# Kernel optimization log

Measured on AMD Instinct MI355X. Metric: run time of the kernel, lower is better.

Reference implementation:

```python
import jax, jax.numpy as jnp
import numpy as np

N_NODES = 50000
N_EDGES = 800000
IN_CH = 64
EDGE_DIM = 8
HIDDEN = 128
NUM_GRAPHS = 256


def setup_inputs() -> dict:
    key = jax.random.key(0)
    ks = jax.random.split(key, 16)
    x = jax.random.normal(ks[0], (N_NODES, IN_CH), dtype=jnp.float32)
    edge_index = jax.random.randint(ks[1], (2, N_EDGES), 0, N_NODES, dtype=jnp.int64)
    edge_attr = jax.random.normal(ks[2], (N_EDGES, EDGE_DIM), dtype=jnp.float32)
    batch = jnp.sort(jax.random.randint(ks[3], (N_NODES,), 0, NUM_GRAPHS, dtype=jnp.int64))

    def lin(k, fan_in, fan_out):
        bound = 1.0 / np.sqrt(fan_in)
        kw, kb = jax.random.split(k)
        W = jax.random.uniform(kw, (fan_in, fan_out), minval=-bound, maxval=bound, dtype=jnp.float32)
        b = jax.random.uniform(kb, (fan_out,), minval=-bound, maxval=bound, dtype=jnp.float32)
        return W, b

    W1, b1 = lin(ks[4], IN_CH, HIDDEN)
    We1, be1 = lin(ks[5], EDGE_DIM, IN_CH)
    W2, b2 = lin(ks[6], HIDDEN, HIDDEN)
    We2, be2 = lin(ks[7], EDGE_DIM, HIDDEN)
    W3, b3 = lin(ks[8], HIDDEN, HIDDEN)
    We3, be3 = lin(ks[9], EDGE_DIM, HIDDEN)
    return {"x": x, "edge_index": edge_index, "edge_attr": edge_attr, "batch": batch,
            "W1": W1, "b1": b1, "We1": We1, "be1": be1,
            "W2": W2, "b2": b2, "We2": We2, "be2": be2,
            "W3": W3, "b3": b3, "We3": We3, "be3": be3}


def gine_conv(x, src, dst, edge_attr, W, b, We, be):
    # edge feature projection to node-feature dim, then message = relu(x_j + e)
    e = edge_attr @ We + be                      # [E, d]
    msg = jax.nn.relu(x[src] + e)                # [E, d]
    agg = jax.ops.segment_sum(msg, dst, num_segments=x.shape[0])  # [N, d]
    # eps = 0 (PyG default, not trainable)
    return (x + agg) @ W + b


def reference(x, edge_index, edge_attr, batch,
              W1, b1, We1, be1, W2, b2, We2, be2, W3, b3, We3, be3):
    x = x.astype(jnp.float32)
    edge_attr = edge_attr.astype(jnp.float32)
    src, dst = edge_index[0], edge_index[1]
    x = jax.nn.relu(gine_conv(x, src, dst, edge_attr, W1, b1, We1, be1))
    x = jax.nn.relu(gine_conv(x, src, dst, edge_attr, W2, b2, We2, be2))
    x = jax.nn.relu(gine_conv(x, src, dst, edge_attr, W3, b3, We3, be3))
    # global mean pool over graphs
    sums = jax.ops.segment_sum(x, batch, num_segments=NUM_GRAPHS)          # [G, d]
    counts = jax.ops.segment_sum(jnp.ones((x.shape[0],), x.dtype), batch, num_segments=NUM_GRAPHS)
    return sums / jnp.maximum(counts, 1.0)[:, None]
```

## Files before the change

### kernel.cpp

```cpp
#include <hip/hip_runtime.h>
#include <hip/hip_bf16.h>
#include <hip/hip_fp16.h>

#define N_NODES 50000
#define N_EDGES 800000
#define IN_CH 64
#define EDGE_DIM 8
#define HIDDEN 128
#define NUM_GRAPHS 256
#define QSCALE 256.0f
#define QINV   (1.0f / 256.0f)

typedef __attribute__((ext_vector_type(8))) _Float16 half8;
typedef __attribute__((ext_vector_type(4))) float floatx4;
typedef __attribute__((ext_vector_type(2))) float floatx2;
typedef __attribute__((ext_vector_type(4))) int intx4;

static __device__ __forceinline__ __half2 u2h(int u) {
    union { int i; __half2 h; } cv; cv.i = u; return cv.h;
}
static __device__ __forceinline__ int h2u(__half2 h) {
    union { __half2 h; int i; } cv; cv.h = h; return cv.i;
}
static __device__ __forceinline__ unsigned short h1u(__half h) {
    union { __half h; unsigned short u; } cv; cv.h = h; return cv.u;
}
static __device__ __forceinline__ unsigned char f32_to_fp8(float v) {
    int pk = __builtin_amdgcn_cvt_pk_fp8_f32(v, v, 0, false);
    return (unsigned char)(pk & 0xff);
}

#define XH_ELEMS (N_NODES * IN_CH)

__global__ __launch_bounds__(256) void hist_cvt_kernel(
    const int* __restrict__ dst, int* __restrict__ deg,
    const float* __restrict__ x, unsigned char* __restrict__ xh8,
    const float* __restrict__ W1, const float* __restrict__ W2,
    const float* __restrict__ W3,
    _Float16* __restrict__ Wt1, _Float16* __restrict__ Wt2,
    _Float16* __restrict__ Wt3, int E)
{
    int i = blockIdx.x * blockDim.x + threadIdx.x;
    if (i < E) atomicAdd(&deg[dst[i]], 1);
    int idx = i;
    if (idx < XH_ELEMS) { xh8[idx] = f32_to_fp8(x[idx]); return; }
    idx -= XH_ELEMS;
    if (idx < 128 * IN_CH) {
        int n = idx / IN_CH, k = idx - n * IN_CH;
        Wt1[idx] = (_Float16)W1[k * 128 + n];
        return;
    }
    idx -= 128 * IN_CH;
    if (idx < 128 * HIDDEN) {
        int n = idx / HIDDEN, k = idx - n * HIDDEN;
        Wt2[idx] = (_Float16)W2[k * 128 + n];
        return;
    }
    idx -= 128 * HIDDEN;
    if (idx < 128 * HIDDEN) {
        int n = idx / HIDDEN, k = idx - n * HIDDEN;
        Wt3[idx] = (_Float16)W3[k * 128 + n];
    }
}

__global__ __launch_bounds__(256) void scan1_kernel(
    const int* __restrict__ deg, int* __restrict__ incl,
    int* __restrict__ blockSums, int N)
{
    __shared__ int s[256];
    int b = blockIdx.x, t = threadIdx.x;
    int i0 = b * 512 + 2 * t;
    int a0 = (i0 < N) ? deg[i0] : 0;
    int a1 = (i0 + 1 < N) ? deg[i0 + 1] : 0;
    int ps = a0 + a1;
    s[t] = ps;
    __syncthreads();
    for (int off = 1; off < 256; off <<= 1) {
        int v = (t >= off) ? s[t - off] : 0;
        __syncthreads();
        s[t] += v;
        __syncthreads();
    }
    int exclp = s[t] - ps;
    if (i0 < N)     incl[i0]     = exclp + a0;
    if (i0 + 1 < N) incl[i0 + 1] = exclp + a0 + a1;
    if (t == 255) blockSums[b] = s[255];
}

__global__ __launch_bounds__(128) void scan2_kernel(int* __restrict__ blockSums, int B)
{
    __shared__ int s[128];
    int t = threadIdx.x;
    int v = (t < B) ? blockSums[t] : 0;
    s[t] = v;
    __syncthreads();
    for (int off = 1; off < 128; off <<= 1) {
        int u = (t >= off) ? s[t - off] : 0;
        __syncthreads();
        s[t] += u;
        __syncthreads();
    }
    if (t < B) blockSums[t] = s[t] - v;
}

__global__ __launch_bounds__(256) void scan3_kernel(
    const int* __restrict__ incl, const int* __restrict__ deg,
    const int* __restrict__ blockSums, int* __restrict__ rowptr,
    int* __restrict__ pos, int N)
{
    int i = blockIdx.x * blockDim.x + threadIdx.x;
    if (i >= N) return;
    int v = incl[i] - deg[i] + blockSums[i >> 9];
    rowptr[i] = v;
    pos[i] = v;
}

__global__ __launch_bounds__(256) void scatter_rec_kernel(
    const int* __restrict__ dst, const int* __restrict__ src,
    const float* __restrict__ ea, int* __restrict__ pos,
    int* __restrict__ rec, int E)
{
    int e = blockIdx.x * blockDim.x + threadIdx.x;
    if (e >= E) return;
    int d = dst[e];
    int p = atomicAdd(&pos[d], 1);
    const float4* q = (const float4*)(ea + (size_t)e * EDGE_DIM);
    float4 a = q[0], b = q[1];
    intx4 r;
    r.x = src[e];
    r.y = h2u(__floats2half2_rn(a.x, a.y));
    r.z = h2u(__floats2half2_rn(a.z, a.w));
    r.w = h2u(__floats2half2_rn(b.x, b.y));
    int* rp = rec + (size_t)p * 8;
    __builtin_nontemporal_store(r, (intx4*)rp);
    __builtin_nontemporal_store(h2u(__floats2half2_rn(b.z, b.w)), rp + 4);
}

#define BF 8

__global__ __launch_bounds__(256) void gather_xs128_kernel(
    const unsigned char* __restrict__ h8,
    const int*    __restrict__ rec,
    const int*    __restrict__ rowptr,
    const int*    __restrict__ deg,
    const float*  __restrict__ We,
    const float*  __restrict__ be,
    __half*       __restrict__ xs,
    int N)
{
    int wave = threadIdx.x >> 6;
    int n    = blockIdx.x * 4 + wave;
    if (n >= N) return;
    int l  = threadIdx.x & 63;
    int j0 = 2 * l;

    __half2 hw[8];
    #pragma unroll
    for (int k = 0; k < 8; ++k) {
        float2 wv = *(const float2*)&We[k * 128 + j0];
        hw[k] = __floats2half2_rn(wv.x, wv.y);
    }
    float2 bevf = *(const float2*)&be[j0];
    __half2 bev2 = __floats2half2_rn(bevf.x, bevf.y);

    int start = __builtin_amdgcn_readfirstlane(rowptr[n]);
    int dg    = __builtin_amdgcn_readfirstlane(deg[n]);

    unsigned short selfraw = *(const unsigned short*)&h8[(size_t)n * 128 + j0];
    floatx2 hf = __builtin_amdgcn_cvt_pk_f32_fp8((int)selfraw, false);
    int acci0 = 0, acci1 = 0;

    int nb = dg / BF;
    int base = start;
    for (int b = 0; b < nb; ++b, base += BF) {
        intx4 r0[BF]; int r1[BF];
        #pragma unroll
        for (int t = 0; t < BF; ++t)
            r0[t] = __builtin_nontemporal_load(
                (const intx4*)&rec[(size_t)(base + t) * 8]);
        #pragma unroll
        for (int t = 0; t < BF; ++t)
            r1[t] = __builtin_nontemporal_load(&rec[(size_t)(base + t) * 8 + 4]);
        int sid[BF];
        #pragma unroll
        for (int t = 0; t < BF; ++t)
            sid[t] = __builtin_amdgcn_readfirstlane(r0[t].x);
        unsigned short hraw[BF];
        #pragma unroll
        for (int t = 0; t < BF; ++t)
            hraw[t] = *(const unsigned short*)&h8[(size_t)sid[t] * 128 + j0];

        #pragma unroll
        for (int t = 0; t < BF; ++t) {
            __half2 e01 = u2h(r0[t].y), e23 = u2h(r0[t].z);
            __half2 e45 = u2h(r0[t].w), e67 = u2h(r1[t]);
            __half2 m = __hfma2(__low2half2(e01),  hw[0], bev2);
            m = __hfma2(__high2half2(e01), hw[1], m);
            m = __hfma2(__low2half2(e23),  hw[2], m);
            m = __hfma2(__high2half2(e23), hw[3], m);
            m = __hfma2(__low2half2(e45),  hw[4], m);
            m = __hfma2(__high2half2(e45), hw[5], m);
            m = __hfma2(__low2half2(e67),  hw[6], m);
            m = __hfma2(__high2half2(e67), hw[7], m);
            floatx2 hs = __builtin_amdgcn_cvt_pk_f32_fp8((int)hraw[t], false);
            float m0 = __half2float(__low2half(m))  + hs.x;
            float m1 = __half2float(__high2half(m)) + hs.y;
            acci0 += (int)((m0 > 0.0f ? m0 : 0.0f) * QSCALE);
            acci1 += (int)((m1 > 0.0f ? m1 : 0.0f) * QSCALE);
        }
    }
    int end = start + dg;
    for (int idx = base; idx < end; ++idx) {
        intx4 r0 = __builtin_nontemporal_load((const intx4*)&rec[(size_t)idx * 8]);
        int r1v  = __builtin_nontemporal_load(&rec[(size_t)idx * 8 + 4]);
        int s = __builtin_amdgcn_readfirstlane(r0.x);
        unsigned short hr = *(const unsigned short*)&h8[(size_t)s * 128 + j0];
        __half2 e01 = u2h(r0.y), e23 = u2h(r0.z), e45 = u2h(r0.w), e67 = u2h(r1v);
        __half2 m = __hfma2(__low2half2(e01),  hw[0], bev2);
        m = __hfma2(__high2half2(e01), hw[1], m);
        m = __hfma2(__low2half2(e23),  hw[2], m);
        m = __hfma2(__high2half2(e23), hw[3], m);
        m = __hfma2(__low2half2(e45),  hw[4], m);
        m = __hfma2(__high2half2(e45), hw[5], m);
        m = __hfma2(__low2half2(e67),  hw[6], m);
        m = __hfma2(__high2half2(e67), hw[7], m);
        floatx2 hs = __builtin_amdgcn_cvt_pk_f32_fp8((int)hr, false);
        float m0 = __half2float(__low2half(m))  + hs.x;
        float m1 = __half2float(__high2half(m)) + hs.y;
        acci0 += (int)((m0 > 0.0f ? m0 : 0.0f) * QSCALE);
        acci1 += (int)((m1 > 0.0f ? m1 : 0.0f) * QSCALE);
    }
    float acc0 = hf.x + (float)acci0 * QINV;
    float acc1 = hf.y + (float)acci1 * QINV;
    __builtin_nontemporal_store(h2u(__floats2half2_rn(acc0, acc1)),
                                (int*)&xs[(size_t)n * 128 + j0]);
}

__global__ __launch_bounds__(256) void gather_xs64_kernel(
    const unsigned char* __restrict__ h8,
    const int*    __restrict__ rec,
    const int*    __restrict__ rowptr,
    const int*    __restrict__ deg,
    const float*  __restrict__ We,
    const float*  __restrict__ be,
    __half*       __restrict__ xs,
    int N)
{
    int wave = threadIdx.x >> 6;
    int n    = blockIdx.x * 4 + wave;
    if (n >= N) return;
    int j = threadIdx.x & 63;

    __half2 w2[4];
    #pragma unroll
    for (int p = 0; p < 4; ++p)
        w2[p] = __floats2half2_rn(We[(2 * p) * 64 + j], We[(2 * p + 1) * 64 + j]);
    float bej = be[j];

    int start = __builtin_amdgcn_readfirstlane(rowptr[n]);
    int dg    = __builtin_amdgcn_readfirstlane(deg[n]);

    float selff = __builtin_amdgcn_cvt_f32_fp8((int)h8[(size_t)n * 64 + j], 0);
    int acci = 0;

    int nb = dg / BF;
    int base = start;
    for (int b = 0; b < nb; ++b, base += BF) {
        intx4 r0[BF]; int r1[BF];
        #pragma unroll
        for (int t = 0; t < BF; ++t)
            r0[t] = __builtin_nontemporal_load(
                (const intx4*)&rec[(size_t)(base + t) * 8]);
        #pragma unroll
        for (int t = 0; t < BF; ++t)
            r1[t] = __builtin_nontemporal_load(&rec[(size_t)(base + t) * 8 + 4]);
        int sid[BF];
        #pragma unroll
        for (int t = 0; t < BF; ++t)
            sid[t] = __builtin_amdgcn_readfirstlane(r0[t].x);
        unsigned char hraw[BF];
        #pragma unroll
        for (int t = 0; t < BF; ++t)
            hraw[t] = h8[(size_t)sid[t] * 64 + j];

        #pragma unroll
        for (int t = 0; t < BF; ++t) {
            __half2 d = __hmul2(u2h(r0[t].y), w2[0]);
            d = __hfma2(u2h(r0[t].z), w2[1], d);
            d = __hfma2(u2h(r0[t].w), w2[2], d);
            d = __hfma2(u2h(r1[t]),   w2[3], d);
            float proj = __half2float(__low2half(d)) + __half2float(__high2half(d));
            float hrf = __builtin_amdgcn_cvt_f32_fp8((int)hraw[t], 0);
            float m = hrf + proj + bej;
            acci += (int)((m > 0.0f ? m : 0.0f) * QSCALE);
        }
    }
    int end = start + dg;
    for (int idx = base; idx < end; ++idx) {
        intx4 r0 = __builtin_nontemporal_load((const intx4*)&rec[(size_t)idx * 8]);
        int r1v  = __builtin_nontemporal_load(&rec[(size_t)idx * 8 + 4]);
        int s = __builtin_amdgcn_readfirstlane(r0.x);
        float hrf = __builtin_amdgcn_cvt_f32_fp8((int)h8[(size_t)s * 64 + j], 0);
        __half2 d = __hmul2(u2h(r0.y), w2[0]);
        d = __hfma2(u2h(r0.z), w2[1], d);
        d = __hfma2(u2h(r0.w), w2[2], d);
        d = __hfma2(u2h(r1v),  w2[3], d);
        float proj = __half2float(__low2half(d)) + __half2float(__high2half(d));
        float m = hrf + proj + bej;
        acci += (int)((m > 0.0f ? m : 0.0f) * QSCALE);
    }
    float acc = selff + (float)acci * QINV;
    __builtin_nontemporal_store(h1u(__float2half(acc)),
                                (unsigned short*)&xs[(size_t)n * 64 + j]);
}

template<int K, bool OUT8>
__global__ __launch_bounds__(256) void node_mfma_kernel(
    const _Float16* __restrict__ xs,
    const _Float16* __restrict__ Wt,
    const float*    __restrict__ b,
    _Float16*       __restrict__ out16,
    unsigned char*  __restrict__ out8,
    int N)
{
    int wave  = threadIdx.x >> 6;
    int lane  = threadIdx.x & 63;
    int row16 = lane & 15;
    int quad  = lane >> 4;
    int m0    = (blockIdx.x * 4 + wave) * 32;

    int nA = m0 + row16;        if (nA >= N) nA = N - 1;
    int nB = m0 + 16 + row16;   if (nB >= N) nB = N - 1;

    floatx4 accA[8], accB[8];
    #pragma unroll
    for (int t = 0; t < 8; ++t) { accA[t] = (floatx4)(0.0f); accB[t] = (floatx4)(0.0f); }

    #pragma unroll
    for (int kc = 0; kc < K; kc += 32) {
        half8 a0 = __builtin_nontemporal_load((const half8*)&xs[(size_t)nA * K + kc + quad * 8]);
        half8 a1 = __builtin_nontemporal_load((const half8*)&xs[(size_t)nB * K + kc + quad * 8]);
        #pragma unroll
        for (int t = 0; t < 8; ++t) {
            half8 bf = *(const half8*)&Wt[(size_t)(t * 16 + row16) * K + kc + quad * 8];
            accA[t] = __builtin_amdgcn_mfma_f32_16x16x32_f16(a0, bf, accA[t], 0, 0, 0);
            accB[t] = __builtin_amdgcn_mfma_f32_16x16x32_f16(a1, bf, accB[t], 0, 0, 0);
        }
    }

    #pragma unroll
    for (int t = 0; t < 8; ++t) {
        int col = t * 16 + row16;
        float bj = b[col];
        #pragma unroll
        for (int r = 0; r < 4; ++r) {
            int nodeA = m0 + quad * 4 + r;
            if (nodeA < N) {
                float v = accA[t][r] + bj;
                v = v > 0.0f ? v : 0.0f;
                if (OUT8) out8[(size_t)nodeA * 128 + col] = f32_to_fp8(v);
                else      out16[(size_t)nodeA * 128 + col] = (_Float16)v;
            }
            int nodeB = m0 + 16 + quad * 4 + r;
            if (nodeB < N) {
                float v = accB[t][r] + bj;
                v = v > 0.0f ? v : 0.0f;
                if (OUT8) out8[(size_t)nodeB * 128 + col] = f32_to_fp8(v);
                else      out16[(size_t)nodeB * 128 + col] = (_Float16)v;
            }
        }
    }
}

__global__ __launch_bounds__(256) void pool_kernel(
    const __half* __restrict__ h,
    const int*    __restrict__ batch,
    float*        __restrict__ out,
    int N)
{
    __shared__ int s_lo, s_hi;
    __shared__ float part[4][128];
    int g  = blockIdx.x;
    int t  = threadIdx.x;
    int fp = t & 63;
    int r  = t >> 6;

    if (t == 0) {
        int lo = 0, hi = N;
        while (lo < hi) { int m = (lo + hi) >> 1; if (batch[m] < g) lo = m + 1; else hi = m; }
        s_lo = lo;
        int lo2 = lo, hi2 = N;
        while (lo2 < hi2) { int m = (lo2 + hi2) >> 1; if (batch[m] < g + 1) lo2 = m + 1; else hi2 = m; }
        s_hi = lo2;
    }
    __syncthreads();

    int lo = s_lo, hi = s_hi;
    float a0 = 0.0f, a1 = 0.0f;
    for (int n = lo + r; n < hi; n += 4) {
        float2 f = __half22float2(*(const __half2*)&h[(size_t)n * 128 + 2 * fp]);
        a0 += f.x; a1 += f.y;
    }
    part[r][2 * fp]     = a0;
    part[r][2 * fp + 1] = a1;
    __syncthreads();

    if (r == 0) {
        float s0 = part[0][2 * fp] + part[1][2 * fp] + part[2][2 * fp] + part[3][2 * fp];
        float s1 = part[0][2 * fp + 1] + part[1][2 * fp + 1] + part[2][2 * fp + 1] + part[3][2 * fp + 1];
        float c = (float)(hi - lo);
        float d = c > 1.0f ? c : 1.0f;
        out[g * HIDDEN + 2 * fp]     = s0 / d;
        out[g * HIDDEN + 2 * fp + 1] = s1 / d;
    }
}

extern "C" void kernel_launch(void* const* d_in, const int* in_sizes, int n_in,
                              void* d_out, int out_size, void* d_ws, size_t ws_size,
                              hipStream_t stream)
{
    const float* x   = (const float*)d_in[0];
    const int*   ei  = (const int*)d_in[1];
    const float* ea  = (const float*)d_in[2];
    const int*   bat = (const int*)d_in[3];
    const float* W1  = (const float*)d_in[4];
    const float* b1  = (const float*)d_in[5];
    const float* We1 = (const float*)d_in[6];
    const float* be1 = (const float*)d_in[7];
    const float* W2  = (const float*)d_in[8];
    const float* b2  = (const float*)d_in[9];
    const float* We2 = (const float*)d_in[10];
    const float* be2 = (const float*)d_in[11];
    const float* W3  = (const float*)d_in[12];
    const float* b3  = (const float*)d_in[13];
    const float* We3 = (const float*)d_in[14];
    const float* be3 = (const float*)d_in[15];
    float* out = (float*)d_out;

    const int* src = ei;
    const int* dst = ei + N_EDGES;

    int* deg       = (int*)d_ws;
    int* rowptr    = deg + N_NODES;
    int* pos       = rowptr + N_NODES;
    int* blockSums = pos + N_NODES;
    int* rec       = blockSums + 128;
    __half* xs     = (__half*)(rec + (size_t)N_EDGES * 8);
    __half* h3h    = xs + (size_t)N_NODES * HIDDEN;
    unsigned char* xh8  = (unsigned char*)(h3h + (size_t)N_NODES * HIDDEN);
    unsigned char* h1_8 = xh8 + (size_t)N_NODES * IN_CH;
    unsigned char* h2_8 = h1_8 + (size_t)N_NODES * HIDDEN;
    _Float16* Wt1  = (_Float16*)(h2_8 + (size_t)N_NODES * HIDDEN);
    _Float16* Wt2  = Wt1 + 128 * IN_CH;
    _Float16* Wt3  = Wt2 + 128 * HIDDEN;

    const int BLK = 256;
    const int NB_E = (N_EDGES + BLK - 1) / BLK;
    const int NB_N = (N_NODES + BLK - 1) / BLK;
    const int SCAN_B = (N_NODES + 511) / 512;
    const int MFMA_B = (N_NODES + 127) / 128;
    const int WAVE4_B = (N_NODES + 3) / 4;
    const int CVT_ELEMS = XH_ELEMS + 128 * IN_CH + 2 * 128 * HIDDEN;
    const int NB_HC = (CVT_ELEMS + BLK - 1) / BLK;

    (void)hipMemsetAsync(deg, 0, N_NODES * sizeof(int), stream);
    hist_cvt_kernel<<<NB_HC, BLK, 0, stream>>>(
        dst, deg, x, xh8, W1, W2, W3, Wt1, Wt2, Wt3, N_EDGES);
    scan1_kernel<<<SCAN_B, 256, 0, stream>>>(deg, pos, blockSums, N_NODES);
    scan2_kernel<<<1, 128, 0, stream>>>(blockSums, SCAN_B);
    scan3_kernel<<<NB_N, BLK, 0, stream>>>(pos, deg, blockSums, rowptr, pos, N_NODES);
    scatter_rec_kernel<<<NB_E, BLK, 0, stream>>>(
        dst, src, ea, pos, rec, N_EDGES);

    gather_xs64_kernel<<<WAVE4_B, BLK, 0, stream>>>(
        xh8, rec, rowptr, deg, We1, be1, xs, N_NODES);
    node_mfma_kernel<IN_CH, true><<<MFMA_B, 256, 0, stream>>>(
        (const _Float16*)xs, Wt1, b1, nullptr, h1_8, N_NODES);

    gather_xs128_kernel<<<WAVE4_B, BLK, 0, stream>>>(
        h1_8, rec, rowptr, deg, We2, be2, xs, N_NODES);
    node_mfma_kernel<HIDDEN, true><<<MFMA_B, 256, 0, stream>>>(
        (const _Float16*)xs, Wt2, b2, nullptr, h2_8, N_NODES);

    gather_xs128_kernel<<<WAVE4_B, BLK, 0, stream>>>(
        h2_8, rec, rowptr, deg, We3, be3, xs, N_NODES);
    node_mfma_kernel<HIDDEN, false><<<MFMA_B, 256, 0, stream>>>(
        (const _Float16*)xs, Wt3, b3, (_Float16*)h3h, nullptr, N_NODES);

    pool_kernel<<<NUM_GRAPHS, 256, 0, stream>>>(h3h, bat, out, N_NODES);
}
```

Baseline: 409.2 us.

## Replace per-node atomic CSR scatter with two-pass bucketed scatter

```diff
diff --git a/kernel.cpp b/kernel.cpp
--- a/kernel.cpp
+++ b/kernel.cpp
@@ -10,6 +10,8 @@
 #define NUM_GRAPHS 256
 #define QSCALE 256.0f
 #define QINV   (1.0f / 256.0f)
+#define BKT_W 128
+#define NBKT ((N_NODES + BKT_W - 1) / BKT_W)
 
 typedef __attribute__((ext_vector_type(8))) _Float16 half8;
 typedef __attribute__((ext_vector_type(4))) float floatx4;
@@ -106,34 +108,62 @@
 __global__ __launch_bounds__(256) void scan3_kernel(
     const int* __restrict__ incl, const int* __restrict__ deg,
     const int* __restrict__ blockSums, int* __restrict__ rowptr,
-    int* __restrict__ pos, int N)
+    int* __restrict__ bcur, int N)
 {
     int i = blockIdx.x * blockDim.x + threadIdx.x;
     if (i >= N) return;
     int v = incl[i] - deg[i] + blockSums[i >> 9];
     rowptr[i] = v;
-    pos[i] = v;
-}
-
-__global__ __launch_bounds__(256) void scatter_rec_kernel(
+    if ((i & (BKT_W - 1)) == 0) bcur[i / BKT_W] = v;
+}
+
+__global__ __launch_bounds__(256) void scatter_stage_kernel(
     const int* __restrict__ dst, const int* __restrict__ src,
-    const float* __restrict__ ea, int* __restrict__ pos,
-    int* __restrict__ rec, int E)
+    const float* __restrict__ ea, int* __restrict__ bcur,
+    int* __restrict__ stage, int E)
 {
     int e = blockIdx.x * blockDim.x + threadIdx.x;
     if (e >= E) return;
     int d = dst[e];
-    int p = atomicAdd(&pos[d], 1);
+    int p = atomicAdd(&bcur[d / BKT_W], 1);
     const float4* q = (const float4*)(ea + (size_t)e * EDGE_DIM);
     float4 a = q[0], b = q[1];
     intx4 r;
-    r.x = src[e];
-    r.y = h2u(__floats2half2_rn(a.x, a.y));
-    r.z = h2u(__floats2half2_rn(a.z, a.w));
-    r.w = h2u(__floats2half2_rn(b.x, b.y));
-    int* rp = rec + (size_t)p * 8;
-    __builtin_nontemporal_store(r, (intx4*)rp);
-    __builtin_nontemporal_store(h2u(__floats2half2_rn(b.z, b.w)), rp + 4);
+    r.x = d;
+    r.y = src[e];
+    r.z = h2u(__floats2half2_rn(a.x, a.y));
+    r.w = h2u(__floats2half2_rn(a.z, a.w));
+    int* sp = stage + (size_t)p * 8;
+    __builtin_nontemporal_store(r, (intx4*)sp);
+    __builtin_nontemporal_store(h2u(__floats2half2_rn(b.x, b.y)), sp + 4);
+    __builtin_nontemporal_store(h2u(__floats2half2_rn(b.z, b.w)), sp + 5);
+}
+
+__global__ __launch_bounds__(256) void scatter_final_kernel(
+    const int* __restrict__ rowptr, const int* __restrict__ stage,
+    int* __restrict__ rec, int N, int E)
+{
+    __shared__ int lpos[BKT_W];
+    int b = blockIdx.x, t = threadIdx.x;
+    int nlo = b * BKT_W;
+    int nhi = nlo + BKT_W; if (nhi > N) nhi = N;
+    int cnt = nhi - nlo;
+    if (t < cnt) lpos[t] = rowptr[nlo + t];
+    int estart = rowptr[nlo];
+    int eend = (nhi < N) ? rowptr[nhi] : E;
+    __syncthreads();
+
+    for (int i = estart + t; i < eend; i += 256) {
+        const int* sp = stage + (size_t)i * 8;
+        intx4 r0 = *(const intx4*)sp;
+        int e45 = sp[4], e67 = sp[5];
+        int slot = atomicAdd(&lpos[r0.x - nlo], 1);
+        intx4 w;
+        w.x = r0.y; w.y = r0.z; w.z = r0.w; w.w = e45;
+        int* rp = rec + (size_t)slot * 8;
+        __builtin_nontemporal_store(w, (intx4*)rp);
+        __builtin_nontemporal_store(e67, rp + 4);
+    }
 }
 
 #define BF 8
@@ -442,9 +472,11 @@
 
     int* deg       = (int*)d_ws;
     int* rowptr    = deg + N_NODES;
-    int* pos       = rowptr + N_NODES;
-    int* blockSums = pos + N_NODES;
-    int* rec       = blockSums + 128;
+    int* incl      = rowptr + N_NODES;
+    int* bcur      = incl + N_NODES;
+    int* blockSums = bcur + 512;
+    int* stage     = blockSums + 128;
+    int* rec       = stage + (size_t)N_EDGES * 8;
     __half* xs     = (__half*)(rec + (size_t)N_EDGES * 8);
     __half* h3h    = xs + (size_t)N_NODES * HIDDEN;
     unsigned char* xh8  = (unsigned char*)(h3h + (size_t)N_NODES * HIDDEN);
@@ -466,11 +498,13 @@
     (void)hipMemsetAsync(deg, 0, N_NODES * sizeof(int), stream);
     hist_cvt_kernel<<<NB_HC, BLK, 0, stream>>>(
         dst, deg, x, xh8, W1, W2, W3, Wt1, Wt2, Wt3, N_EDGES);
-    scan1_kernel<<<SCAN_B, 256, 0, stream>>>(deg, pos, blockSums, N_NODES);
+    scan1_kernel<<<SCAN_B, 256, 0, stream>>>(deg, incl, blockSums, N_NODES);
     scan2_kernel<<<1, 128, 0, stream>>>(blockSums, SCAN_B);
-    scan3_kernel<<<NB_N, BLK, 0, stream>>>(pos, deg, blockSums, rowptr, pos, N_NODES);
-    scatter_rec_kernel<<<NB_E, BLK, 0, stream>>>(
-        dst, src, ea, pos, rec, N_EDGES);
+    scan3_kernel<<<NB_N, BLK, 0, stream>>>(incl, deg, blockSums, rowptr, bcur, N_NODES);
+    scatter_stage_kernel<<<NB_E, BLK, 0, stream>>>(
+        dst, src, ea, bcur, stage, N_EDGES);
+    scatter_final_kernel<<<NBKT, BLK, 0, stream>>>(
+        rowptr, stage, rec, N_NODES, N_EDGES);
 
     gather_xs64_kernel<<<WAVE4_B, BLK, 0, stream>>>(
         xh8, rec, rowptr, deg, We1, be1, xs, N_NODES);
```

Result: slower. 676.2 us (+65.3%).
